# Kernel tuning notes

Hardware: AMD Instinct MI355X
Metric: run time of the kernel (lower is better)

Reference implementation:

```python
import jax, jax.numpy as jnp
import numpy as np

B, L, D, Z, H, N, G = 8, 2048, 1024, 128, 2048, 16, 32
MAXPOS = 2048
EPS = 1e-5
PRIOR_COUNT = 2.0  # TimestepNorm prior pseudo-count


def setup_inputs() -> dict:
    ks = jax.random.split(jax.random.key(0), 12)
    std = 0.02  # bert init
    return {
        "x": jax.random.normal(ks[0], (B, L, D), jnp.float32),
        "prior_mean": jnp.zeros((G,), jnp.float32),
        "prior_logv": jnp.zeros((G,), jnp.float32),
        "tn_weight": jnp.ones((D,), jnp.float32),
        "tn_bias": jnp.zeros((D,), jnp.float32),
        "delta": jax.random.normal(ks[1], (D, N), jnp.float32),
        "alpha": jax.random.normal(ks[2], (D, N), jnp.float32),
        "ema_beta": jax.random.normal(ks[3], (D, N), jnp.float32),
        "ema_gamma": jax.random.normal(ks[4], (D, N), jnp.float32),
        "omega": jax.random.normal(ks[5], (D,), jnp.float32),
        "rms_weight": jnp.ones((D,), jnp.float32),
        "Wv": jax.random.normal(ks[6], (H, D), jnp.float32) * std,
        "bv": jnp.zeros((H,), jnp.float32),
        "Wmx": jax.random.normal(ks[7], (Z + H + 2 * D, D), jnp.float32) * std,
        "bmx": jnp.zeros((Z + H + 2 * D,), jnp.float32),
        "Wh": jax.random.normal(ks[8], (D, H), jnp.float32) * std,
        "qk_gamma": jax.random.normal(ks[9], (2, Z), jnp.float32) * 0.1,
        "qk_beta": jax.random.normal(ks[10], (2, Z), jnp.float32) * 0.1,
        "rel_bias": jax.random.normal(ks[11], (2 * MAXPOS - 1,), jnp.float32) * 0.02,
    }


def timestep_norm(x, prior_mean, prior_logv, weight, bias):
    """Causal cumulative group norm with a prior (TimestepNorm)."""
    m = D // G  # features per group
    xg = x.reshape(B, L, G, m)
    s1 = jnp.cumsum(xg.sum(-1), axis=1)            # B,L,G  running sum
    s2 = jnp.cumsum((xg * xg).sum(-1), axis=1)     # B,L,G  running sum of squares
    cnt = PRIOR_COUNT + m * jnp.arange(1, L + 1, dtype=x.dtype)[None, :, None]
    pv = jnp.exp(prior_logv)
    mean = (PRIOR_COUNT * prior_mean + s1) / cnt
    var = (PRIOR_COUNT * (pv + prior_mean ** 2) + s2) / cnt - mean ** 2
    xn = (xg - mean[..., None]) * jax.lax.rsqrt(var[..., None] + EPS)
    return xn.reshape(B, L, D) * weight + bias


def multihead_ema(x, delta, alpha, ema_beta, ema_gamma, omega):
    """MultiHeadEMA: causal damped-EMA convolution via FFT, plus omega residual."""
    p = jax.nn.sigmoid(delta)                       # D,N
    a = jax.nn.sigmoid(alpha)
    q = 1.0 - p * a                                 # decay in (0,1)
    t = jnp.arange(L, dtype=x.dtype)
    vander = jnp.exp(t[None, None, :] * jnp.log(q)[:, :, None])  # D,N,L
    scale = 1.0 / jnp.sqrt(jnp.asarray(N, x.dtype))
    kern = jnp.einsum('dn,dnl,dn->dl', p * ema_beta, vander, ema_gamma * scale)
    xT = x.transpose(0, 2, 1)                       # B,D,L
    n = 2 * L
    out = jnp.fft.irfft(jnp.fft.rfft(xT, n=n) * jnp.fft.rfft(kern, n=n)[None], n=n)[..., :L]
    out = out + xT * omega[:, None]
    return out.transpose(0, 2, 1)


def _forward(x, prior_mean, prior_logv, tn_weight, tn_bias, delta, alpha,
             ema_beta, ema_gamma, omega, rms_weight, Wv, bv, Wmx, bmx, Wh,
             qk_gamma, qk_beta, rel_bias):
    residual = x
    xn = timestep_norm(x, prior_mean, prior_logv, tn_weight, tn_bias)
    v = jax.nn.silu(xn @ Wv.T + bv)                 # B,L,H
    mx = multihead_ema(xn, delta, alpha, ema_beta, ema_gamma, omega)
    mx = mx * jax.lax.rsqrt(jnp.mean(mx * mx, axis=-1, keepdims=True) + EPS) * rms_weight  # RMSNorm
    base = mx @ Wmx.T + bmx                         # B,L,Z+H+2D
    u = jax.nn.sigmoid(base[..., :D])
    zr = jax.nn.silu(base[..., D:D + Z + H])
    hx = base[..., D + Z + H:]
    z, r = zr[..., :Z], zr[..., Z:]
    zz = z[..., None, :] * qk_gamma + qk_beta       # B,L,2,Z
    q = zz[..., 0, :] * (Z ** -0.5)
    k = zz[..., 1, :]
    # simple relative positional bias: bias[i,j] = rel_bias[MAXPOS-1 + (j-i)]
    idx = (MAXPOS - 1) + (jnp.arange(L)[None, :] - jnp.arange(L)[:, None])
    qk = jnp.einsum('biz,bjz->bij', q, k) + rel_bias[idx]
    causal = jnp.tril(jnp.ones((L, L), bool))
    qk = jnp.where(causal, qk, -jnp.inf)
    attn = jax.nn.softmax(qk, axis=-1)              # B,L,L
    h = jnp.einsum('bij,bjh->bih', attn, v)         # B,L,H
    h = jax.nn.silu(hx + (h * r) @ Wh.T)            # B,L,D
    return residual + u * (h - residual)


def reference(x, prior_mean, prior_logv, tn_weight, tn_bias, delta, alpha,
              ema_beta, ema_gamma, omega, rms_weight, Wv, bv, Wmx, bmx, Wh,
              qk_gamma, qk_beta, rel_bias):
    return _forward(x, prior_mean, prior_logv, tn_weight, tn_bias, delta, alpha,
                    ema_beta, ema_gamma, omega, rms_weight, Wv, bv, Wmx, bmx, Wh,
                    qk_gamma, qk_beta, rel_bias)
```

## Files before the change

### kernel.cpp

```cpp
#include <hip/hip_runtime.h>
#include <stdint.h>

#define B_ 8
#define L_ 2048
#define D_ 1024
#define Z_ 128
#define H_ 2048
#define NE_ 16
#define G_ 32
#define MAXPOS_ 2048
#define NMX_ 4224
#define EPS_ 1e-5f
#define PC_ 2.0f
#define NTILE_ 16
#define NPACK_ 136
#define TILE_ELEMS_ 16384

typedef short bf16x8 __attribute__((ext_vector_type(8)));
typedef float f32x4 __attribute__((ext_vector_type(4)));

__device__ __forceinline__ float bf2f(uint16_t u) {
  union { uint32_t u; float f; } v; v.u = ((uint32_t)u) << 16; return v.f;
}
__device__ __forceinline__ uint16_t f2bf(float f) {
  union { float f; uint32_t u; } v; v.f = f;
  uint32_t r = (v.u + 0x7FFFu + ((v.u >> 16) & 1u)) >> 16;
  return (uint16_t)r;
}
__device__ __forceinline__ float sigmoidf_(float x) { return 1.f / (1.f + __expf(-x)); }
__device__ __forceinline__ float siluf_(float x) { return x / (1.f + __expf(-x)); }

__device__ __forceinline__ float waveRedSum(float v) {
  #pragma unroll
  for (int m = 32; m; m >>= 1) v += __shfl_xor(v, m, 64);
  return v;
}

__device__ __forceinline__ void gl2lds(const uint16_t* g, uint16_t* l) {
  __builtin_amdgcn_global_load_lds(
      (const __attribute__((address_space(1))) void*)g,
      (__attribute__((address_space(3))) void*)l, 16, 0, 0);
}

__global__ __launch_bounds__(256) void k_fallback(float* __restrict__ out, int n, float wsmb) {
  for (int i = blockIdx.x * 256 + threadIdx.x; i < n; i += gridDim.x * 256)
    out[i] = (i == 0) ? wsmb : 0.f;
}

__global__ __launch_bounds__(256) void k_f2bf(const float* __restrict__ src,
                                              uint16_t* __restrict__ dst, int n) {
  for (int i = blockIdx.x * 256 + threadIdx.x; i < n; i += gridDim.x * 256)
    dst[i] = f2bf(src[i]);
}

__global__ __launch_bounds__(256) void k_tnsum(const float* __restrict__ x,
                                               float* __restrict__ s1g,
                                               float* __restrict__ s2g) {
  const int bg = blockIdx.x;
  const int b = bg / G_, g = bg % G_;
  const int tid = threadIdx.x;
  const int j = tid & 31;
  const int lsub = tid >> 5;
  #pragma unroll
  for (int i = 0; i < 16; ++i) {
    const int l = blockIdx.y * 128 + i * 8 + lsub;
    float v = x[((size_t)(b * L_ + l)) * D_ + g * 32 + j];
    float a = v, sq = v * v;
    #pragma unroll
    for (int m = 1; m <= 16; m <<= 1) { a += __shfl_xor(a, m, 64); sq += __shfl_xor(sq, m, 64); }
    if (j == 0) { s1g[(size_t)bg * L_ + l] = a; s2g[(size_t)bg * L_ + l] = sq; }
  }
}

__global__ __launch_bounds__(64) void k_tnscan(float* __restrict__ s1g,
                                               float* __restrict__ s2g) {
  const int bg = blockIdx.x;
  const int lane = threadIdx.x;
  #pragma unroll
  for (int pass = 0; pass < 2; ++pass) {
    float* gp = (pass ? s2g : s1g) + (size_t)bg * L_;
    float loc[32];
    const int b0 = lane * 32;
    float tot = 0.f;
    #pragma unroll
    for (int t = 0; t < 32; ++t) { loc[t] = gp[b0 + t]; tot += loc[t]; }
    float incl = tot;
    #pragma unroll
    for (int off = 1; off < 64; off <<= 1) {
      float nv = __shfl_up(incl, off, 64);
      if (lane >= off) incl += nv;
    }
    float run = incl - tot;
    #pragma unroll
    for (int t = 0; t < 32; ++t) { run += loc[t]; gp[b0 + t] = run; }
  }
}

__global__ __launch_bounds__(256) void k_tnnorm(const float* __restrict__ x,
                                                const float* __restrict__ s1g,
                                                const float* __restrict__ s2g,
                                                const float* __restrict__ pm,
                                                const float* __restrict__ plv,
                                                const float* __restrict__ w,
                                                const float* __restrict__ bias,
                                                uint16_t* __restrict__ xn) {
  const int bg = blockIdx.x;
  const int b = bg / G_, g = bg % G_;
  const int tid = threadIdx.x;
  const int j = tid & 31;
  const int lsub = tid >> 5;
  const float pmv = pm[g];
  const float pvv = __expf(plv[g]);
  const float wj = w[g * 32 + j];
  const float bj = bias[g * 32 + j];
  const float pterm = PC_ * (pvv + pmv * pmv);
  #pragma unroll
  for (int i = 0; i < 16; ++i) {
    const int l = blockIdx.y * 128 + i * 8 + lsub;
    const size_t idx = ((size_t)(b * L_ + l)) * D_ + g * 32 + j;
    const float v = x[idx];
    const float cnt = PC_ + 32.f * (float)(l + 1);
    const float mean = (PC_ * pmv + s1g[(size_t)bg * L_ + l]) / cnt;
    const float var = (pterm + s2g[(size_t)bg * L_ + l]) / cnt - mean * mean;
    xn[idx] = f2bf((v - mean) * rsqrtf(var + EPS_) * wj + bj);
  }
}

__global__ __launch_bounds__(256) void k_tp16(const uint16_t* __restrict__ src,
                                              uint16_t* __restrict__ dst, int R, int C) {
  __shared__ uint16_t tile[64 * 65];
  const size_t batch = (size_t)R * C * blockIdx.z;
  const int c0 = blockIdx.x * 64, r0 = blockIdx.y * 64;
  const int t = threadIdx.x;
  const int rr = t >> 3;
  const int cc = (t & 7) * 8;
  #pragma unroll
  for (int p = 0; p < 2; ++p) {
    const int row = p * 32 + rr;
    bf16x8 v = *(const bf16x8*)&src[batch + (size_t)(r0 + row) * C + c0 + cc];
    #pragma unroll
    for (int i = 0; i < 8; ++i) tile[(cc + i) * 65 + row] = (uint16_t)v[i];
  }
  __syncthreads();
  #pragma unroll
  for (int p = 0; p < 2; ++p) {
    const int crow = p * 32 + rr;
    bf16x8 o;
    #pragma unroll
    for (int i = 0; i < 8; ++i) o[i] = (short)tile[crow * 65 + cc + i];
    *(bf16x8*)&dst[batch + (size_t)(c0 + crow) * R + r0 + cc] = o;
  }
}

__global__ __launch_bounds__(256) void k_tpf32(const float* __restrict__ src,
                                               float* __restrict__ dst, int R, int C) {
  __shared__ float tile[64 * 65];
  const size_t batch = (size_t)R * C * blockIdx.z;
  const int c0 = blockIdx.x * 64, r0 = blockIdx.y * 64;
  const int t = threadIdx.x;
  const int rr = t >> 4;
  const int cc = (t & 15) * 4;
  #pragma unroll
  for (int p = 0; p < 4; ++p) {
    const int row = p * 16 + rr;
    f32x4 v = *(const f32x4*)&src[batch + (size_t)(r0 + row) * C + c0 + cc];
    #pragma unroll
    for (int i = 0; i < 4; ++i) tile[(cc + i) * 65 + row] = v[i];
  }
  __syncthreads();
  #pragma unroll
  for (int p = 0; p < 4; ++p) {
    const int crow = p * 16 + rr;
    f32x4 o;
    #pragma unroll
    for (int i = 0; i < 4; ++i) o[i] = tile[crow * 65 + cc + i];
    *(f32x4*)&dst[batch + (size_t)(c0 + crow) * R + r0 + cc] = o;
  }
}

__global__ __launch_bounds__(64) void k_ema(const uint16_t* __restrict__ xnT,
                                            const float* __restrict__ delta,
                                            const float* __restrict__ alpha,
                                            const float* __restrict__ beta,
                                            const float* __restrict__ gamma,
                                            const float* __restrict__ omega,
                                            float* __restrict__ mxT) {
  __shared__ float hst[64 * NE_];
  const int bd = blockIdx.x;
  const int d = bd & (D_ - 1);
  const int c = threadIdx.x;

  float q[NE_], pb[NE_], gs[NE_];
  #pragma unroll
  for (int n = 0; n < NE_; ++n) {
    float p = sigmoidf_(delta[d * NE_ + n]);
    float a = sigmoidf_(alpha[d * NE_ + n]);
    q[n] = 1.f - p * a;
    pb[n] = p * beta[d * NE_ + n];
    gs[n] = gamma[d * NE_ + n] * 0.25f;
  }

  const uint16_t* xp = xnT + (size_t)bd * L_ + c * 32;
  bf16x8 xin[4];
  #pragma unroll
  for (int s = 0; s < 4; ++s) xin[s] = *(const bf16x8*)(xp + s * 8);

  float h[NE_];
  #pragma unroll
  for (int n = 0; n < NE_; ++n) h[n] = 0.f;

  #pragma unroll
  for (int k = 0; k < 32; ++k) {
    float xv = bf2f((uint16_t)xin[k >> 3][k & 7]);
    #pragma unroll
    for (int n = 0; n < NE_; ++n) h[n] = fmaf(q[n], h[n], pb[n] * xv);
  }
  #pragma unroll
  for (int n = 0; n < NE_; ++n) hst[c * NE_ + n] = h[n];
  __syncthreads();

  if (c < NE_) {
    float qq = q[c];
    float q32 = qq * qq; q32 *= q32; q32 *= q32; q32 *= q32; q32 *= q32;
    float hi = 0.f;
    for (int cc = 0; cc < 64; ++cc) {
      float cur = hst[cc * NE_ + c];
      hst[cc * NE_ + c] = hi;
      hi = fmaf(q32, hi, cur);
    }
  }
  __syncthreads();

  #pragma unroll
  for (int n = 0; n < NE_; ++n) h[n] = hst[c * NE_ + n];
  const float om = omega[d];
  float* op = mxT + (size_t)bd * L_ + c * 32;
  f32x4 ov;
  #pragma unroll
  for (int k = 0; k < 32; ++k) {
    float xv = bf2f((uint16_t)xin[k >> 3][k & 7]);
    float accv = 0.f;
    #pragma unroll
    for (int n = 0; n < NE_; ++n) {
      h[n] = fmaf(q[n], h[n], pb[n] * xv);
      accv = fmaf(gs[n], h[n], accv);
    }
    ov[k & 3] = accv + om * xv;
    if ((k & 3) == 3) *(f32x4*)(op + (k & ~3)) = ov;
  }
}

__global__ __launch_bounds__(256) void k_rms(const float* __restrict__ mx,
                                             const float* __restrict__ w,
                                             uint16_t* __restrict__ mxn) {
  __shared__ float red[4];
  const size_t row = blockIdx.x;
  const int tid = threadIdx.x;
  float ss = 0.f;
  #pragma unroll
  for (int i = 0; i < 4; ++i) {
    float v = mx[row * D_ + tid + i * 256];
    ss += v * v;
  }
  ss = waveRedSum(ss);
  if ((tid & 63) == 0) red[tid >> 6] = ss;
  __syncthreads();
  ss = red[0] + red[1] + red[2] + red[3];
  const float scale = rsqrtf(ss * (1.f / D_) + EPS_);
  #pragma unroll
  for (int i = 0; i < 4; ++i) {
    int dcol = tid + i * 256;
    mxn[row * D_ + dcol] = f2bf(mx[row * D_ + dcol] * scale * w[dcol]);
  }
}

__global__ __launch_bounds__(256) void k_qkprep(const float* __restrict__ z,
                                                const float* __restrict__ qg,
                                                const float* __restrict__ qb,
                                                uint16_t* __restrict__ q,
                                                uint16_t* __restrict__ k, int n) {
  for (int i = blockIdx.x * 256 + threadIdx.x; i < n; i += gridDim.x * 256) {
    int zc = i & (Z_ - 1);
    float v = z[i];
    q[i] = f2bf((v * qg[zc] + qb[zc]) * 0.08838834764831845f);
    k[i] = f2bf(v * qg[Z_ + zc] + qb[Z_ + zc]);
  }
}


template <int MODE>
__global__ __launch_bounds__(256, 4) void k_gemm128(
    const uint16_t* __restrict__ A, const uint16_t* __restrict__ Bm,
    int N, int K,
    const float* __restrict__ bias,
    float* __restrict__ outf, uint16_t* __restrict__ outb,
    uint16_t* __restrict__ ubuf, float* __restrict__ zbuf,
    uint16_t* __restrict__ rbuf, float* __restrict__ hxbuf,
    const float* __restrict__ x0) {
  __shared__ uint16_t sm[17408];
  const int t = threadIdx.x;
  const int lane = t & 63, wave = t >> 6;
  const int quad = lane >> 4, r16 = lane & 15;
  const int wm = wave >> 1, wn = wave & 1;
  const int bm = blockIdx.x * 128;
  const int bn = blockIdx.y * 128;

  f32x4 acc[4][4];
  const f32x4 zf = {0.f, 0.f, 0.f, 0.f};
  #pragma unroll
  for (int i = 0; i < 4; ++i)
    #pragma unroll
    for (int j = 0; j < 4; ++j) acc[i][j] = zf;

  const int sgz = (((t & 3) ^ ((t >> 3) & 3)) << 3);
  const uint16_t* gA = A + (size_t)(bm + (t >> 2)) * K + sgz;
  const uint16_t* gB = Bm + (size_t)(bn + (t >> 2)) * K + sgz;
  const size_t qstep = (size_t)64 * K;
  uint16_t* lA = sm + t * 8;
  uint16_t* lB = sm + 4096 + t * 8;

  const int ga = ((quad ^ ((r16 >> 1) & 3)) << 3);
  const int aOff = (wm * 64 + r16) * 32 + ga;
  const int bOff = 4096 + (wn * 64 + r16) * 32 + ga;

#define STAGE(c, kb) do {                                                     \
    gl2lds(gA + (kb), lA + (c) * 8192);                                       \
    gl2lds(gA + qstep + (kb), lA + (c) * 8192 + 2048);                        \
    gl2lds(gB + (kb), lB + (c) * 8192);                                       \
    gl2lds(gB + qstep + (kb), lB + (c) * 8192 + 2048);                        \
  } while (0)

  const int NT = K >> 5;

  STAGE(0, 0);
  __syncthreads();

  bf16x8 af[4], bfr[4];
  for (int tt = 0; tt < NT; ++tt) {
    const int c = tt & 1;
    const int co = c * 8192;
    if (tt + 1 < NT) STAGE(c ^ 1, (tt + 1) * 32);
    #pragma unroll
    for (int j = 0; j < 4; ++j)
      bfr[j] = *(const bf16x8*)&sm[co + bOff + j * 512];
    #pragma unroll
    for (int i = 0; i < 4; ++i)
      af[i] = *(const bf16x8*)&sm[co + aOff + i * 512];
    #pragma unroll
    for (int i = 0; i < 4; ++i)
      #pragma unroll
      for (int j = 0; j < 4; ++j)
        acc[i][j] = __builtin_amdgcn_mfma_f32_16x16x32_bf16(
            af[i], bfr[j], acc[i][j], 0, 0, 0);
    __syncthreads();
  }
#undef STAGE

  if (MODE == 0) {
    #pragma unroll
    for (int i = 0; i < 4; ++i)
      #pragma unroll
      for (int j = 0; j < 4; ++j)
        #pragma unroll
        for (int r = 0; r < 4; ++r) {
          const int hloc = wn * 64 + j * 16 + r16;
          const int lloc = wm * 64 + i * 16 + quad * 4 + r;
          sm[hloc * 136 + lloc] = f2bf(siluf_(acc[i][j][r] + bias[bn + hloc]));
        }
    __syncthreads();
    const int bb = bm >> 11;
    const int lb = bm & 2047;
    uint16_t* vTb = outb + (size_t)bb * H_ * L_;
    #pragma unroll
    for (int p = 0; p < 8; ++p) {
      const int hloc = p * 16 + (t >> 4);
      const int l0 = (t & 15) * 8;
      bf16x8 v = *(const bf16x8*)&sm[hloc * 136 + l0];
      *(bf16x8*)&vTb[(size_t)(bn + hloc) * L_ + lb + l0] = v;
    }
  } else {
    #pragma unroll
    for (int i = 0; i < 4; ++i) {
      #pragma unroll
      for (int j = 0; j < 4; ++j) {
        #pragma unroll
        for (int r = 0; r < 4; ++r) {
          const int row = bm + wm * 64 + i * 16 + quad * 4 + r;
          const int col = bn + wn * 64 + j * 16 + r16;
          float val = acc[i][j][r];
          if (MODE == 1) {
            val += bias[col];
            if (col < D_)                 ubuf[(size_t)row * D_ + col] = f2bf(sigmoidf_(val));
            else if (col < D_ + Z_)       zbuf[(size_t)row * Z_ + (col - D_)] = siluf_(val);
            else if (col < D_ + Z_ + H_)  rbuf[(size_t)row * H_ + (col - D_ - Z_)] = f2bf(siluf_(val));
            else                          hxbuf[(size_t)row * D_ + (col - D_ - Z_ - H_)] = val;
          } else {
            const size_t idx = (size_t)row * N + col;
            float g = siluf_(val + hxbuf[idx]);
            float xv = x0[idx];
            outf[idx] = xv + bf2f(ubuf[idx]) * (g - xv);
          }
        }
      }
    }
  }
}

__global__ __launch_bounds__(256) void k_qksm(
    const uint16_t* __restrict__ qg, const uint16_t* __restrict__ kg,
    const float* __restrict__ relb, uint16_t* __restrict__ Pp) {
  __shared__ uint16_t Ks[128 * 128];
  __shared__ float relwin[256];
  const int qt = blockIdx.x;
  const int bl = blockIdx.y;
  const int tid = threadIdx.x;
  const int w = tid >> 6, lane = tid & 63;
  const int quad = lane >> 4, r16 = lane & 15;
  const uint16_t* qb_b = qg + (size_t)bl * L_ * Z_;
  const uint16_t* kb_b = kg + (size_t)bl * L_ * Z_;
  uint16_t* P_b = Pp + (size_t)bl * NPACK_ * TILE_ELEMS_;

  const int ksg = (tid >> 4) * 128 + (((tid & 15) ^ ((tid >> 4) & 7)) << 3);
  const int kg7 = r16 & 7;

  bf16x8 aq[2][4];
  #pragma unroll
  for (int i = 0; i < 2; ++i)
    #pragma unroll
    for (int s = 0; s < 4; ++s)
      aq[i][s] = *(const bf16x8*)&qb_b[(size_t)(qt * 128 + w * 32 + i * 16 + r16) * Z_ +
                                       s * 32 + quad * 8];

  float m8[8], l8[8];
  #pragma unroll
  for (int t = 0; t < 8; ++t) { m8[t] = -3.4e38f; l8[t] = 0.f; }

  const f32x4 zf = {0.f, 0.f, 0.f, 0.f};

  for (int kt = 0; kt <= qt; ++kt) {
    __syncthreads();
    const uint16_t* src = kb_b + (size_t)kt * 128 * Z_;
    #pragma unroll
    for (int s2 = 0; s2 < 8; ++s2)
      gl2lds(src + s2 * 2048 + ksg, Ks + s2 * 2048 + tid * 8);
    if (tid < 255) relwin[tid] = relb[2047 + (kt - qt) * 128 - 127 + tid];
    __syncthreads();
    #pragma unroll
    for (int j = 0; j < 8; ++j) {
      f32x4 a0 = zf, a1 = zf;
      #pragma unroll
      for (int s = 0; s < 4; ++s) {
        bf16x8 bk = *(const bf16x8*)&Ks[(j * 16 + r16) * 128 +
                                        (((s * 4 + quad) ^ kg7) << 3)];
        a0 = __builtin_amdgcn_mfma_f32_16x16x32_bf16(aq[0][s], bk, a0, 0, 0, 0);
        a1 = __builtin_amdgcn_mfma_f32_16x16x32_bf16(aq[1][s], bk, a1, 0, 0, 0);
      }
      #pragma unroll
      for (int i = 0; i < 2; ++i) {
        const f32x4 av = i ? a1 : a0;
        #pragma unroll
        for (int r = 0; r < 4; ++r) {
          const int rloc = w * 32 + i * 16 + quad * 4 + r;
          const int cloc = j * 16 + r16;
          if (kt < qt || cloc <= rloc) {
            const float v = av[r] + relwin[cloc - rloc + 127];
            const int t = i * 4 + r;
            const float mn = fmaxf(m8[t], v);
            l8[t] = l8[t] * __expf(m8[t] - mn) + __expf(v - mn);
            m8[t] = mn;
          }
        }
      }
    }
  }

  #pragma unroll
  for (int t = 0; t < 8; ++t) {
    #pragma unroll
    for (int msk = 1; msk <= 8; msk <<= 1) {
      const float mo = __shfl_xor(m8[t], msk, 64);
      const float lo = __shfl_xor(l8[t], msk, 64);
      const float mn = fmaxf(m8[t], mo);
      l8[t] = l8[t] * __expf(m8[t] - mn) + lo * __expf(mo - mn);
      m8[t] = mn;
    }
    l8[t] = 1.f / l8[t];
  }

  for (int kt = 0; kt <= qt; ++kt) {
    __syncthreads();
    const uint16_t* src = kb_b + (size_t)kt * 128 * Z_;
    #pragma unroll
    for (int s2 = 0; s2 < 8; ++s2)
      gl2lds(src + s2 * 2048 + ksg, Ks + s2 * 2048 + tid * 8);
    if (tid < 255) relwin[tid] = relb[2047 + (kt - qt) * 128 - 127 + tid];
    __syncthreads();
    uint16_t* Pt = P_b + (size_t)(qt * (qt + 1) / 2 + kt) * TILE_ELEMS_;
    #pragma unroll
    for (int j = 0; j < 8; ++j) {
      f32x4 a0 = zf, a1 = zf;
      #pragma unroll
      for (int s = 0; s < 4; ++s) {
        bf16x8 bk = *(const bf16x8*)&Ks[(j * 16 + r16) * 128 +
                                        (((s * 4 + quad) ^ kg7) << 3)];
        a0 = __builtin_amdgcn_mfma_f32_16x16x32_bf16(aq[0][s], bk, a0, 0, 0, 0);
        a1 = __builtin_amdgcn_mfma_f32_16x16x32_bf16(aq[1][s], bk, a1, 0, 0, 0);
      }
      #pragma unroll
      for (int i = 0; i < 2; ++i) {
        const f32x4 av = i ? a1 : a0;
        #pragma unroll
        for (int r = 0; r < 4; ++r) {
          const int rloc = w * 32 + i * 16 + quad * 4 + r;
          const int cloc = j * 16 + r16;
          const int t = i * 4 + r;
          float p = 0.f;
          if (kt < qt || cloc <= rloc) {
            const float v = av[r] + relwin[cloc - rloc + 127];
            p = __expf(v - m8[t]) * l8[t];
          }
          Pt[rloc * 128 + cloc] = f2bf(p);
        }
      }
    }
  }
}

__global__ __launch_bounds__(256, 4) void k_pv(
    const uint16_t* __restrict__ Pp, const uint16_t* __restrict__ vT,
    uint16_t* __restrict__ rh) {
  __shared__ uint16_t sm[16384];
  const int qt = NTILE_ - 1 - blockIdx.x;
  const int bn = blockIdx.y * 128;
  const int bl = blockIdx.z;
  const uint16_t* Pq = Pp + (size_t)bl * NPACK_ * TILE_ELEMS_ +
                       (size_t)(qt * (qt + 1) / 2) * TILE_ELEMS_;
  const uint16_t* v_b = vT + (size_t)bl * H_ * L_;
  uint16_t* rh_b = rh + (size_t)bl * L_ * H_;

  const int tid = threadIdx.x;
  const int wave = tid >> 6, lane = tid & 63;
  const int quad = lane >> 4, r16 = lane & 15;
  const int wm = wave >> 1, wn = wave & 1;
  const int rowW = wm * 64, colW = wn * 64;

  f32x4 acc[4][4];
  const f32x4 zf = {0.f, 0.f, 0.f, 0.f};
  #pragma unroll
  for (int i = 0; i < 4; ++i)
    #pragma unroll
    for (int j = 0; j < 4; ++j) acc[i][j] = zf;

  const int rA = tid >> 2;
  const int sg = (((tid & 3) ^ ((tid >> 3) & 3)) << 3);
  const int gpv = ((quad ^ ((r16 >> 1) & 3)) << 3);

#define PVSTAGE(c, s) do {                                                    \
    const int kt_ = (s) >> 2, ks_ = (s) & 3;                                  \
    const uint16_t* At_ = Pq + (size_t)kt_ * TILE_ELEMS_ + ks_ * 32 + sg;     \
    const uint16_t* Bt_ = v_b + (size_t)(bn + rA) * L_ + kt_ * 128 +          \
                          ks_ * 32 + sg;                                      \
    gl2lds(At_ + rA * 128, sm + (c) * 8192 + tid * 8);                        \
    gl2lds(At_ + (rA + 64) * 128, sm + (c) * 8192 + 2048 + tid * 8);          \
    gl2lds(Bt_, sm + (c) * 8192 + 4096 + tid * 8);                            \
    gl2lds(Bt_ + (size_t)64 * L_, sm + (c) * 8192 + 6144 + tid * 8);          \
  } while (0)

  const int S = 4 * (qt + 1);

  PVSTAGE(0, 0);
  __syncthreads();

  bf16x8 af[4], bfr[4];
  for (int s = 0; s < S; ++s) {
    const int c = s & 1;
    const int co = c * 8192;
    if (s + 1 < S) PVSTAGE(c ^ 1, s + 1);
    #pragma unroll
    for (int j = 0; j < 4; ++j)
      bfr[j] = *(const bf16x8*)&sm[co + 4096 + (colW + j * 16 + r16) * 32 + gpv];
    #pragma unroll
    for (int i = 0; i < 4; ++i)
      af[i] = *(const bf16x8*)&sm[co + (rowW + i * 16 + r16) * 32 + gpv];
    #pragma unroll
    for (int i = 0; i < 4; ++i)
      #pragma unroll
      for (int j = 0; j < 4; ++j)
        acc[i][j] = __builtin_amdgcn_mfma_f32_16x16x32_bf16(af[i], bfr[j], acc[i][j], 0, 0, 0);
    __syncthreads();
  }
#undef PVSTAGE

  #pragma unroll
  for (int i = 0; i < 4; ++i) {
    #pragma unroll
    for (int j = 0; j < 4; ++j) {
      #pragma unroll
      for (int r = 0; r < 4; ++r) {
        const int row = qt * 128 + rowW + i * 16 + quad * 4 + r;
        const int col = bn + colW + j * 16 + r16;
        const size_t idx = (size_t)row * H_ + col;
        const float rv = bf2f(rh_b[idx]);
        rh_b[idx] = f2bf(acc[i][j][r] * rv);
      }
    }
  }
}

extern "C" void kernel_launch(void* const* d_in, const int* in_sizes, int n_in,
                              void* d_out, int out_size, void* d_ws, size_t ws_size,
                              hipStream_t stream) {
  (void)in_sizes; (void)n_in;
  const float* x         = (const float*)d_in[0];
  const float* prior_mean= (const float*)d_in[1];
  const float* prior_logv= (const float*)d_in[2];
  const float* tn_w      = (const float*)d_in[3];
  const float* tn_b      = (const float*)d_in[4];
  const float* delta     = (const float*)d_in[5];
  const float* alpha     = (const float*)d_in[6];
  const float* ema_beta  = (const float*)d_in[7];
  const float* ema_gamma = (const float*)d_in[8];
  const float* omega     = (const float*)d_in[9];
  const float* rms_w     = (const float*)d_in[10];
  const float* Wv        = (const float*)d_in[11];
  const float* bv        = (const float*)d_in[12];
  const float* Wmx       = (const float*)d_in[13];
  const float* bmx       = (const float*)d_in[14];
  const float* Wh        = (const float*)d_in[15];
  const float* qk_gamma  = (const float*)d_in[16];
  const float* qk_beta   = (const float*)d_in[17];
  const float* rel_bias  = (const float*)d_in[18];
  float* out = (float*)d_out;

  const int BL = B_ * L_;
  const size_t MB = 1024 * 1024;
  const size_t REQUIRED = 256 * MB;

  if (ws_size < REQUIRED) {
    k_fallback<<<dim3(4096), dim3(256), 0, stream>>>(out, out_size, (float)(ws_size / MB));
    return;
  }

  char* p = (char*)d_ws;
  uint16_t* xn   = (uint16_t*)(p);
  uint16_t* ubuf = (uint16_t*)(p);
  float*    s1g  = (float*)   (p + 32 * MB);
  float*    s2g  = (float*)   (p + 34 * MB);
  uint16_t* xnT  = (uint16_t*)(p + 32 * MB);
  uint16_t* mxn  = (uint16_t*)(p + 32 * MB);
  uint16_t* vT   = (uint16_t*)(p + 64 * MB);
  uint16_t* wv_b = (uint16_t*)(p + 128 * MB);
  float*    mx   = (float*)   (p + 128 * MB);
  uint16_t* rbuf = (uint16_t*)(p + 128 * MB);
  uint16_t* wmx_b = (uint16_t*)(p + 192 * MB);
  uint16_t* wh_b  = (uint16_t*)(p + 192 * MB);
  float*    zb    = (float*)   (p + 201 * MB);
  uint16_t* qb    = (uint16_t*)(p + 209 * MB);
  uint16_t* kb2   = (uint16_t*)(p + 213 * MB);
  uint16_t* Ppack = (uint16_t*)(p + 217 * MB);
  float* mxT = out;
  float* hx  = out;

  k_f2bf<<<dim3(1024), dim3(256), 0, stream>>>(Wv, wv_b, H_ * D_);
  k_f2bf<<<dim3(2048), dim3(256), 0, stream>>>(Wmx, wmx_b, NMX_ * D_);
  k_tnsum<<<dim3(B_ * G_, 16), dim3(256), 0, stream>>>(x, s1g, s2g);
  k_tnscan<<<dim3(B_ * G_), dim3(64), 0, stream>>>(s1g, s2g);
  k_tnnorm<<<dim3(B_ * G_, 16), dim3(256), 0, stream>>>(
      x, s1g, s2g, prior_mean, prior_logv, tn_w, tn_b, xn);
  k_tp16<<<dim3(D_ / 64, L_ / 64, B_), dim3(256), 0, stream>>>(xn, xnT, L_, D_);
  k_gemm128<0><<<dim3(BL / 128, H_ / 128), dim3(256), 0, stream>>>(
      xn, wv_b, H_, D_, bv, nullptr, vT,
      nullptr, nullptr, nullptr, nullptr, nullptr);
  k_ema<<<dim3(B_ * D_), dim3(64), 0, stream>>>(xnT, delta, alpha, ema_beta, ema_gamma, omega, mxT);
  k_tpf32<<<dim3(L_ / 64, D_ / 64, B_), dim3(256), 0, stream>>>(mxT, mx, D_, L_);
  k_rms<<<dim3(BL), dim3(256), 0, stream>>>(mx, rms_w, mxn);
  k_gemm128<1><<<dim3(BL / 128, NMX_ / 128), dim3(256), 0, stream>>>(
      mxn, wmx_b, NMX_, D_, bmx, nullptr, nullptr,
      ubuf, zb, rbuf, hx, nullptr);
  k_qkprep<<<dim3(1024), dim3(256), 0, stream>>>(zb, qk_gamma, qk_beta, qb, kb2, BL * Z_);
  k_qksm<<<dim3(NTILE_, B_), dim3(256), 0, stream>>>(qb, kb2, rel_bias, Ppack);
  k_pv<<<dim3(NTILE_, H_ / 128, B_), dim3(256), 0, stream>>>(Ppack, vT, rbuf);
  k_f2bf<<<dim3(1024), dim3(256), 0, stream>>>(Wh, wh_b, D_ * H_);
  k_gemm128<4><<<dim3(BL / 128, D_ / 128), dim3(256), 0, stream>>>(
      rbuf, wh_b, D_, H_, nullptr, out, nullptr,
      ubuf, nullptr, nullptr, hx, x);
}
```

Measured before the change: 1.158 ms.

## Fuse qk prep into gemm epilogue, double-buffer K tiles, widen PV blocks

```diff
diff --git a/kernel.cpp b/kernel.cpp
--- a/kernel.cpp
+++ b/kernel.cpp
@@ -274,19 +274,6 @@
   }
 }
 
-__global__ __launch_bounds__(256) void k_qkprep(const float* __restrict__ z,
-                                                const float* __restrict__ qg,
-                                                const float* __restrict__ qb,
-                                                uint16_t* __restrict__ q,
-                                                uint16_t* __restrict__ k, int n) {
-  for (int i = blockIdx.x * 256 + threadIdx.x; i < n; i += gridDim.x * 256) {
-    int zc = i & (Z_ - 1);
-    float v = z[i];
-    q[i] = f2bf((v * qg[zc] + qb[zc]) * 0.08838834764831845f);
-    k[i] = f2bf(v * qg[Z_ + zc] + qb[Z_ + zc]);
-  }
-}
-
 
 template <int MODE>
 __global__ __launch_bounds__(256, 4) void k_gemm128(
@@ -294,9 +281,11 @@
     int N, int K,
     const float* __restrict__ bias,
     float* __restrict__ outf, uint16_t* __restrict__ outb,
-    uint16_t* __restrict__ ubuf, float* __restrict__ zbuf,
+    uint16_t* __restrict__ ubuf,
     uint16_t* __restrict__ rbuf, float* __restrict__ hxbuf,
-    const float* __restrict__ x0) {
+    const float* __restrict__ x0,
+    const float* __restrict__ qkg, const float* __restrict__ qkb,
+    uint16_t* __restrict__ qbuf, uint16_t* __restrict__ kbuf) {
   __shared__ uint16_t sm[17408];
   const int t = threadIdx.x;
   const int lane = t & 63, wave = t >> 6;
@@ -390,10 +379,20 @@
           float val = acc[i][j][r];
           if (MODE == 1) {
             val += bias[col];
-            if (col < D_)                 ubuf[(size_t)row * D_ + col] = f2bf(sigmoidf_(val));
-            else if (col < D_ + Z_)       zbuf[(size_t)row * Z_ + (col - D_)] = siluf_(val);
-            else if (col < D_ + Z_ + H_)  rbuf[(size_t)row * H_ + (col - D_ - Z_)] = f2bf(siluf_(val));
-            else                          hxbuf[(size_t)row * D_ + (col - D_ - Z_ - H_)] = val;
+            if (col < D_) {
+              ubuf[(size_t)row * D_ + col] = f2bf(sigmoidf_(val));
+            } else if (col < D_ + Z_) {
+              const int zc = col - D_;
+              const float zv = siluf_(val);
+              qbuf[(size_t)row * Z_ + zc] =
+                  f2bf((zv * qkg[zc] + qkb[zc]) * 0.08838834764831845f);
+              kbuf[(size_t)row * Z_ + zc] =
+                  f2bf(zv * qkg[Z_ + zc] + qkb[Z_ + zc]);
+            } else if (col < D_ + Z_ + H_) {
+              rbuf[(size_t)row * H_ + (col - D_ - Z_)] = f2bf(siluf_(val));
+            } else {
+              hxbuf[(size_t)row * D_ + (col - D_ - Z_ - H_)] = val;
+            }
           } else {
             const size_t idx = (size_t)row * N + col;
             float g = siluf_(val + hxbuf[idx]);
@@ -409,8 +408,8 @@
 __global__ __launch_bounds__(256) void k_qksm(
     const uint16_t* __restrict__ qg, const uint16_t* __restrict__ kg,
     const float* __restrict__ relb, uint16_t* __restrict__ Pp) {
-  __shared__ uint16_t Ks[128 * 128];
-  __shared__ float relwin[256];
+  __shared__ uint16_t Ks[2 * 16384];
+  __shared__ float relwin[2 * 256];
   const int qt = blockIdx.x;
   const int bl = blockIdx.y;
   const int tid = threadIdx.x;
@@ -423,6 +422,15 @@
   const int ksg = (tid >> 4) * 128 + (((tid & 15) ^ ((tid >> 4) & 7)) << 3);
   const int kg7 = r16 & 7;
 
+#define STGK(c, kt) do {                                                      \
+    const uint16_t* src_ = kb_b + (size_t)(kt) * 128 * Z_;                    \
+    _Pragma("unroll")                                                         \
+    for (int s2 = 0; s2 < 8; ++s2)                                            \
+      gl2lds(src_ + s2 * 2048 + ksg, Ks + (c) * 16384 + s2 * 2048 + tid * 8); \
+    if (tid < 255)                                                            \
+      relwin[(c) * 256 + tid] = relb[2047 + ((kt) - qt) * 128 - 127 + tid];   \
+  } while (0)
+
   bf16x8 aq[2][4];
   #pragma unroll
   for (int i = 0; i < 2; ++i)
@@ -437,20 +445,19 @@
 
   const f32x4 zf = {0.f, 0.f, 0.f, 0.f};
 
+  STGK(0, 0);
+  __syncthreads();
   for (int kt = 0; kt <= qt; ++kt) {
-    __syncthreads();
-    const uint16_t* src = kb_b + (size_t)kt * 128 * Z_;
-    #pragma unroll
-    for (int s2 = 0; s2 < 8; ++s2)
-      gl2lds(src + s2 * 2048 + ksg, Ks + s2 * 2048 + tid * 8);
-    if (tid < 255) relwin[tid] = relb[2047 + (kt - qt) * 128 - 127 + tid];
-    __syncthreads();
+    const int cur = kt & 1;
+    if (kt < qt) STGK(cur ^ 1, kt + 1);
+    const uint16_t* Kc = Ks + cur * 16384;
+    const float* rw = relwin + cur * 256;
     #pragma unroll
     for (int j = 0; j < 8; ++j) {
       f32x4 a0 = zf, a1 = zf;
       #pragma unroll
       for (int s = 0; s < 4; ++s) {
-        bf16x8 bk = *(const bf16x8*)&Ks[(j * 16 + r16) * 128 +
+        bf16x8 bk = *(const bf16x8*)&Kc[(j * 16 + r16) * 128 +
                                         (((s * 4 + quad) ^ kg7) << 3)];
         a0 = __builtin_amdgcn_mfma_f32_16x16x32_bf16(aq[0][s], bk, a0, 0, 0, 0);
         a1 = __builtin_amdgcn_mfma_f32_16x16x32_bf16(aq[1][s], bk, a1, 0, 0, 0);
@@ -463,7 +470,7 @@
           const int rloc = w * 32 + i * 16 + quad * 4 + r;
           const int cloc = j * 16 + r16;
           if (kt < qt || cloc <= rloc) {
-            const float v = av[r] + relwin[cloc - rloc + 127];
+            const float v = av[r] + rw[cloc - rloc + 127];
             const int t = i * 4 + r;
             const float mn = fmaxf(m8[t], v);
             l8[t] = l8[t] * __expf(m8[t] - mn) + __expf(v - mn);
@@ -472,6 +479,7 @@
         }
       }
     }
+    __syncthreads();
   }
 
   #pragma unroll
@@ -487,21 +495,20 @@
     l8[t] = 1.f / l8[t];
   }
 
+  STGK(0, 0);
+  __syncthreads();
   for (int kt = 0; kt <= qt; ++kt) {
-    __syncthreads();
-    const uint16_t* src = kb_b + (size_t)kt * 128 * Z_;
-    #pragma unroll
-    for (int s2 = 0; s2 < 8; ++s2)
-      gl2lds(src + s2 * 2048 + ksg, Ks + s2 * 2048 + tid * 8);
-    if (tid < 255) relwin[tid] = relb[2047 + (kt - qt) * 128 - 127 + tid];
-    __syncthreads();
+    const int cur = kt & 1;
+    if (kt < qt) STGK(cur ^ 1, kt + 1);
+    const uint16_t* Kc = Ks + cur * 16384;
+    const float* rw = relwin + cur * 256;
     uint16_t* Pt = P_b + (size_t)(qt * (qt + 1) / 2 + kt) * TILE_ELEMS_;
     #pragma unroll
     for (int j = 0; j < 8; ++j) {
       f32x4 a0 = zf, a1 = zf;
       #pragma unroll
       for (int s = 0; s < 4; ++s) {
-        bf16x8 bk = *(const bf16x8*)&Ks[(j * 16 + r16) * 128 +
+        bf16x8 bk = *(const bf16x8*)&Kc[(j * 16 + r16) * 128 +
                                         (((s * 4 + quad) ^ kg7) << 3)];
         a0 = __builtin_amdgcn_mfma_f32_16x16x32_bf16(aq[0][s], bk, a0, 0, 0, 0);
         a1 = __builtin_amdgcn_mfma_f32_16x16x32_bf16(aq[1][s], bk, a1, 0, 0, 0);
@@ -516,22 +523,24 @@
           const int t = i * 4 + r;
           float p = 0.f;
           if (kt < qt || cloc <= rloc) {
-            const float v = av[r] + relwin[cloc - rloc + 127];
+            const float v = av[r] + rw[cloc - rloc + 127];
             p = __expf(v - m8[t]) * l8[t];
           }
           Pt[rloc * 128 + cloc] = f2bf(p);
         }
       }
     }
-  }
-}
-
-__global__ __launch_bounds__(256, 4) void k_pv(
+    __syncthreads();
+  }
+#undef STGK
+}
+
+__global__ __launch_bounds__(512, 4) void k_pv(
     const uint16_t* __restrict__ Pp, const uint16_t* __restrict__ vT,
     uint16_t* __restrict__ rh) {
-  __shared__ uint16_t sm[16384];
+  __shared__ uint16_t sm[24576];
   const int qt = NTILE_ - 1 - blockIdx.x;
-  const int bn = blockIdx.y * 128;
+  const int bn = blockIdx.y * 256;
   const int bl = blockIdx.z;
   const uint16_t* Pq = Pp + (size_t)bl * NPACK_ * TILE_ELEMS_ +
                        (size_t)(qt * (qt + 1) / 2) * TILE_ELEMS_;
@@ -541,7 +550,7 @@
   const int tid = threadIdx.x;
   const int wave = tid >> 6, lane = tid & 63;
   const int quad = lane >> 4, r16 = lane & 15;
-  const int wm = wave >> 1, wn = wave & 1;
+  const int wm = wave >> 2, wn = wave & 3;
   const int rowW = wm * 64, colW = wn * 64;
 
   f32x4 acc[4][4];
@@ -557,13 +566,12 @@
 
 #define PVSTAGE(c, s) do {                                                    \
     const int kt_ = (s) >> 2, ks_ = (s) & 3;                                  \
-    const uint16_t* At_ = Pq + (size_t)kt_ * TILE_ELEMS_ + ks_ * 32 + sg;     \
+    gl2lds(Pq + (size_t)kt_ * TILE_ELEMS_ + rA * 128 + ks_ * 32 + sg,         \
+           sm + (c) * 12288 + tid * 8);                                       \
     const uint16_t* Bt_ = v_b + (size_t)(bn + rA) * L_ + kt_ * 128 +          \
                           ks_ * 32 + sg;                                      \
-    gl2lds(At_ + rA * 128, sm + (c) * 8192 + tid * 8);                        \
-    gl2lds(At_ + (rA + 64) * 128, sm + (c) * 8192 + 2048 + tid * 8);          \
-    gl2lds(Bt_, sm + (c) * 8192 + 4096 + tid * 8);                            \
-    gl2lds(Bt_ + (size_t)64 * L_, sm + (c) * 8192 + 6144 + tid * 8);          \
+    gl2lds(Bt_, sm + (c) * 12288 + 4096 + tid * 8);                           \
+    gl2lds(Bt_ + (size_t)128 * L_, sm + (c) * 12288 + 8192 + tid * 8);        \
   } while (0)
 
   const int S = 4 * (qt + 1);
@@ -574,7 +582,7 @@
   bf16x8 af[4], bfr[4];
   for (int s = 0; s < S; ++s) {
     const int c = s & 1;
-    const int co = c * 8192;
+    const int co = c * 12288;
     if (s + 1 < S) PVSTAGE(c ^ 1, s + 1);
     #pragma unroll
     for (int j = 0; j < 4; ++j)
@@ -654,7 +662,6 @@
   uint16_t* rbuf = (uint16_t*)(p + 128 * MB);
   uint16_t* wmx_b = (uint16_t*)(p + 192 * MB);
   uint16_t* wh_b  = (uint16_t*)(p + 192 * MB);
-  float*    zb    = (float*)   (p + 201 * MB);
   uint16_t* qb    = (uint16_t*)(p + 209 * MB);
   uint16_t* kb2   = (uint16_t*)(p + 213 * MB);
   uint16_t* Ppack = (uint16_t*)(p + 217 * MB);
@@ -670,18 +677,17 @@
   k_tp16<<<dim3(D_ / 64, L_ / 64, B_), dim3(256), 0, stream>>>(xn, xnT, L_, D_);
   k_gemm128<0><<<dim3(BL / 128, H_ / 128), dim3(256), 0, stream>>>(
       xn, wv_b, H_, D_, bv, nullptr, vT,
-      nullptr, nullptr, nullptr, nullptr, nullptr);
+      nullptr, nullptr, nullptr, nullptr, nullptr, nullptr, nullptr, nullptr);
   k_ema<<<dim3(B_ * D_), dim3(64), 0, stream>>>(xnT, delta, alpha, ema_beta, ema_gamma, omega, mxT);
   k_tpf32<<<dim3(L_ / 64, D_ / 64, B_), dim3(256), 0, stream>>>(mxT, mx, D_, L_);
   k_rms<<<dim3(BL), dim3(256), 0, stream>>>(mx, rms_w, mxn);
   k_gemm128<1><<<dim3(BL / 128, NMX_ / 128), dim3(256), 0, stream>>>(
       mxn, wmx_b, NMX_, D_, bmx, nullptr, nullptr,
-      ubuf, zb, rbuf, hx, nullptr);
-  k_qkprep<<<dim3(1024), dim3(256), 0, stream>>>(zb, qk_gamma, qk_beta, qb, kb2, BL * Z_);
+      ubuf, rbuf, hx, nullptr, qk_gamma, qk_beta, qb, kb2);
   k_qksm<<<dim3(NTILE_, B_), dim3(256), 0, stream>>>(qb, kb2, rel_bias, Ppack);
-  k_pv<<<dim3(NTILE_, H_ / 128, B_), dim3(256), 0, stream>>>(Ppack, vT, rbuf);
+  k_pv<<<dim3(NTILE_, H_ / 256, B_), dim3(512), 0, stream>>>(Ppack, vT, rbuf);
   k_f2bf<<<dim3(1024), dim3(256), 0, stream>>>(Wh, wh_b, D_ * H_);
   k_gemm128<4><<<dim3(BL / 128, D_ / 128), dim3(256), 0, stream>>>(
       rbuf, wh_b, D_, H_, nullptr, out, nullptr,
-      ubuf, nullptr, nullptr, hx, x);
-}
+      ubuf, nullptr, hx, x, nullptr, nullptr, nullptr, nullptr);
+}
```

Measured after the change: 1.153 ms. Within noise of the previous version (-0.4%).
